# Optimization experiments

Hardware: AMD Instinct MI355X
Metric: run time of the kernel (lower is better)

## Reference

```python
import jax, jax.numpy as jnp
import numpy as np

B, S, D = 4, 2048, 512
H = 8
DEPTH = D // H  # 64


def setup_inputs() -> dict:
    key = jax.random.key(0)
    ks = jax.random.split(key, 6)
    scale = 1.0 / np.sqrt(D)
    return {
        "x": jax.random.normal(ks[0], (B, S, D), dtype=jnp.float32),
        "y": jax.random.normal(ks[1], (B, S, D), dtype=jnp.float32),
        "W_q": jax.random.normal(ks[2], (D, D), dtype=jnp.float32) * scale,
        "W_k": jax.random.normal(ks[3], (D, D), dtype=jnp.float32) * scale,
        "W_v": jax.random.normal(ks[4], (D, D), dtype=jnp.float32) * scale,
        "W_o": jax.random.normal(ks[5], (D, D), dtype=jnp.float32) * scale,
    }


def _split_heads(t):
    # [B, S, D] -> [B, H, S, DEPTH]
    b, s, _ = t.shape
    return t.reshape(b, s, H, DEPTH).transpose(0, 2, 1, 3)


def reference(x, y, W_q, W_k, W_v, W_o):
    q = _split_heads(x @ W_q) * (DEPTH ** -0.5)   # [B,H,Sq,d]
    k = _split_heads(y @ W_k)                      # [B,H,Sk,d]
    v = _split_heads(y @ W_v)                      # [B,H,Sk,d]
    logits = jnp.einsum("bhqd,bhkd->bhqk", q, k)   # [B,H,Sq,Sk]
    weights = jax.nn.softmax(logits, axis=-1)
    attn = jnp.einsum("bhqk,bhkd->bhqd", weights, v)  # [B,H,Sq,d]
    attn = attn.transpose(0, 2, 1, 3).reshape(x.shape[0], x.shape[1], D)
    return attn @ W_o
```

## Files before the change

### kernel.cpp

```cpp
#include <hip/hip_runtime.h>
#include <hip/hip_bf16.h>
#include <math.h>
#include <stdint.h>

#define NB 4
#define NS 2048
#define ND 512
#define NH 8
#define DEP 64

typedef __attribute__((ext_vector_type(8))) short bf16x8;
typedef __attribute__((ext_vector_type(4))) short bf16x4;
typedef __attribute__((ext_vector_type(4))) float f32x4;

#define QSCALE 0.18033688011112042f

__device__ __forceinline__ short f2b(float f) {
  unsigned u = __float_as_uint(f);
  u += 0x7FFF + ((u >> 16) & 1);
  return (short)(u >> 16);
}
__device__ __forceinline__ unsigned pk2(float a, float b) {
  union { __hip_bfloat162 h; unsigned u; } c;
  c.h = __float22bfloat162_rn(float2{a, b});
  return c.u;
}
__device__ __forceinline__ void dma16(const void* g, void* l) {
  __builtin_amdgcn_global_load_lds(
      (const __attribute__((address_space(1))) void*)g,
      (__attribute__((address_space(3))) void*)l, 16, 0, 0);
}

__global__ __launch_bounds__(256) void prep(
    const float* __restrict__ x, const float* __restrict__ y,
    const float* __restrict__ W0, const float* __restrict__ W1,
    const float* __restrict__ W2, const float* __restrict__ W3,
    short* __restrict__ xb, short* __restrict__ yb, short* __restrict__ T0,
    short* __restrict__ T1, short* __restrict__ T2, short* __restrict__ T3) {
  const int t = threadIdx.x;
  if (blockIdx.y < 2) {
    const float* src = blockIdx.y ? y : x;
    short* dst = blockIdx.y ? yb : xb;
    size_t i = ((size_t)blockIdx.x * 256 + t) * 4;
    float4 v = *(const float4*)(src + i);
    bf16x4 o;
    o[0] = f2b(v.x); o[1] = f2b(v.y); o[2] = f2b(v.z); o[3] = f2b(v.w);
    *(bf16x4*)(dst + i) = o;
    return;
  }
  const int bx = blockIdx.x;
  if (bx >= 256) return;
  const int wj = bx >> 6, rem = bx & 63;
  const float* W = wj == 0 ? W0 : wj == 1 ? W1 : wj == 2 ? W2 : W3;
  short* T = wj == 0 ? T0 : wj == 1 ? T1 : wj == 2 ? T2 : T3;
  __shared__ float tile[64][65];
  const int k0 = (rem >> 3) * 64, n0 = (rem & 7) * 64;
#pragma unroll
  for (int i = 0; i < 4; ++i) {
    int r = (t >> 4) + i * 16;
    int c = (t & 15) * 4;
    float4 v = *(const float4*)&W[(size_t)(k0 + r) * ND + n0 + c];
    tile[r][c] = v.x; tile[r][c + 1] = v.y;
    tile[r][c + 2] = v.z; tile[r][c + 3] = v.w;
  }
  __syncthreads();
#pragma unroll
  for (int i = 0; i < 4; ++i) {
    int n = (t >> 4) + i * 16;
    int kc = (t & 15) * 4;
    bf16x4 o;
#pragma unroll
    for (int j = 0; j < 4; ++j) o[j] = f2b(tile[kc + j][n]);
    *(bf16x4*)&T[(size_t)(n0 + n) * ND + k0 + kc] = o;
  }
}

__global__ __launch_bounds__(256) void qkv_gemm(
    const short* __restrict__ xb, const short* __restrict__ yb,
    const short* __restrict__ Wqt, const short* __restrict__ Wkt,
    const short* __restrict__ Wvt, short* __restrict__ Qb,
    short* __restrict__ Kb, short* __restrict__ Vtb) {
  __shared__ short As[128 * 64];
  __shared__ short B0s[64 * 64];
  __shared__ short B1s[64 * 64];
  const int z = blockIdx.z;
  const short* A = z ? yb : xb;
  const short* Bt0 = z ? Wkt : Wqt;
  const int t = threadIdx.x;
  const int wave = t >> 6, lane = t & 63;
  const int m = lane & 15, quad = lane >> 4;
  const int m0 = blockIdx.y * 128, n0 = blockIdx.x * 64;
  const int mh = (wave >> 1) * 64, nh = (wave & 1) * 32;
  const int r8 = lane >> 3;
  const int c8 = (lane & 7) ^ r8;
  const int mx7 = m & 7;
  f32x4 acc0[4][2], acc1[4][2];
#pragma unroll
  for (int i = 0; i < 4; ++i)
#pragma unroll
    for (int j = 0; j < 2; ++j) {
      acc0[i][j] = (f32x4){0.f, 0.f, 0.f, 0.f};
      acc1[i][j] = (f32x4){0.f, 0.f, 0.f, 0.f};
    }

  for (int k0 = 0; k0 < ND; k0 += 64) {
    __syncthreads();
#pragma unroll
    for (int i = 0; i < 4; ++i)
      dma16(A + (size_t)(m0 + i * 32 + wave * 8 + r8) * ND + k0 + c8 * 8,
            As + (i * 256 + wave * 64) * 8);
#pragma unroll
    for (int i = 0; i < 2; ++i)
      dma16(Bt0 + (size_t)(n0 + i * 32 + wave * 8 + r8) * ND + k0 + c8 * 8,
            B0s + (i * 256 + wave * 64) * 8);
    if (z) {
#pragma unroll
      for (int i = 0; i < 2; ++i)
        dma16(Wvt + (size_t)(n0 + i * 32 + wave * 8 + r8) * ND + k0 + c8 * 8,
              B1s + (i * 256 + wave * 64) * 8);
    }
    __syncthreads();
    bf16x8 af[4][2], bf0[2][2];
#pragma unroll
    for (int mt = 0; mt < 4; ++mt)
#pragma unroll
      for (int kc = 0; kc < 2; ++kc)
        af[mt][kc] = *(const bf16x8*)(As + (mh + mt * 16 + m) * 64 +
                                      ((kc * 4 + quad) ^ mx7) * 8);
#pragma unroll
    for (int nt = 0; nt < 2; ++nt)
#pragma unroll
      for (int kc = 0; kc < 2; ++kc)
        bf0[nt][kc] = *(const bf16x8*)(B0s + (nh + nt * 16 + m) * 64 +
                                       ((kc * 4 + quad) ^ mx7) * 8);
#pragma unroll
    for (int mt = 0; mt < 4; ++mt)
#pragma unroll
      for (int nt = 0; nt < 2; ++nt)
#pragma unroll
        for (int kc = 0; kc < 2; ++kc)
          acc0[mt][nt] = __builtin_amdgcn_mfma_f32_16x16x32_bf16(
              af[mt][kc], bf0[nt][kc], acc0[mt][nt], 0, 0, 0);
    if (z) {
      bf16x8 bf1[2][2];
#pragma unroll
      for (int nt = 0; nt < 2; ++nt)
#pragma unroll
        for (int kc = 0; kc < 2; ++kc)
          bf1[nt][kc] = *(const bf16x8*)(B1s + (nh + nt * 16 + m) * 64 +
                                         ((kc * 4 + quad) ^ mx7) * 8);
#pragma unroll
      for (int mt = 0; mt < 4; ++mt)
#pragma unroll
        for (int nt = 0; nt < 2; ++nt)
#pragma unroll
          for (int kc = 0; kc < 2; ++kc)
            acc1[mt][nt] = __builtin_amdgcn_mfma_f32_16x16x32_bf16(
                af[mt][kc], bf1[nt][kc], acc1[mt][nt], 0, 0, 0);
    }
  }
  short* C0 = z ? Kb : Qb;
  const float alpha0 = z ? 1.0f : QSCALE;
#pragma unroll
  for (int mt = 0; mt < 4; ++mt)
#pragma unroll
    for (int nt = 0; nt < 2; ++nt)
#pragma unroll
      for (int r = 0; r < 4; ++r) {
        int row = m0 + mh + mt * 16 + quad * 4 + r;
        int col = n0 + nh + nt * 16 + m;
        C0[(size_t)row * ND + col] = f2b(acc0[mt][nt][r] * alpha0);
      }
  if (z) {
#pragma unroll
    for (int mt = 0; mt < 4; ++mt)
#pragma unroll
      for (int nt = 0; nt < 2; ++nt) {
        int row0 = m0 + mh + mt * 16 + quad * 4;
        int col = n0 + nh + nt * 16 + m;
        int b_ = row0 >> 11, s_ = row0 & (NS - 1);
        int h_ = col >> 6, d_ = col & (DEP - 1);
        uint2 p;
        p.x = pk2(acc1[mt][nt][0], acc1[mt][nt][1]);
        p.y = pk2(acc1[mt][nt][2], acc1[mt][nt][3]);
        *(uint2*)(Vtb + (size_t)((b_ * NH + h_) * DEP + d_) * NS + s_) = p;
      }
  }
}

__global__ __launch_bounds__(256) void out_gemm(const short* __restrict__ A,
                                                const short* __restrict__ Bt,
                                                float* __restrict__ Cout) {
  __shared__ short As[2][128 * 64];
  __shared__ short Bs[2][64 * 64];
  const int t = threadIdx.x;
  const int wave = t >> 6, lane = t & 63;
  const int m = lane & 15, quad = lane >> 4;
  const int m0 = blockIdx.y * 128, n0 = blockIdx.x * 64;
  const int mh = (wave >> 1) * 64, nh = (wave & 1) * 32;
  const int r8 = lane >> 3;
  const int c8 = (lane & 7) ^ r8;
  const int mx7 = m & 7;
  f32x4 acc[4][2];
#pragma unroll
  for (int i = 0; i < 4; ++i)
#pragma unroll
    for (int j = 0; j < 2; ++j) acc[i][j] = (f32x4){0.f, 0.f, 0.f, 0.f};

#pragma unroll
  for (int i = 0; i < 4; ++i)
    dma16(A + (size_t)(m0 + i * 32 + wave * 8 + r8) * ND + c8 * 8,
          As[0] + (i * 256 + wave * 64) * 8);
#pragma unroll
  for (int i = 0; i < 2; ++i)
    dma16(Bt + (size_t)(n0 + i * 32 + wave * 8 + r8) * ND + c8 * 8,
          Bs[0] + (i * 256 + wave * 64) * 8);

  int buf = 0;
  for (int k0 = 0; k0 < ND; k0 += 64, buf ^= 1) {
    __syncthreads();
    if (k0 + 64 < ND) {
#pragma unroll
      for (int i = 0; i < 4; ++i)
        dma16(A + (size_t)(m0 + i * 32 + wave * 8 + r8) * ND + k0 + 64 + c8 * 8,
              As[buf ^ 1] + (i * 256 + wave * 64) * 8);
#pragma unroll
      for (int i = 0; i < 2; ++i)
        dma16(Bt + (size_t)(n0 + i * 32 + wave * 8 + r8) * ND + k0 + 64 +
                  c8 * 8,
              Bs[buf ^ 1] + (i * 256 + wave * 64) * 8);
    }
    bf16x8 af[4][2], bf[2][2];
#pragma unroll
    for (int mt = 0; mt < 4; ++mt)
#pragma unroll
      for (int kc = 0; kc < 2; ++kc)
        af[mt][kc] = *(const bf16x8*)(As[buf] + (mh + mt * 16 + m) * 64 +
                                      ((kc * 4 + quad) ^ mx7) * 8);
#pragma unroll
    for (int nt = 0; nt < 2; ++nt)
#pragma unroll
      for (int kc = 0; kc < 2; ++kc)
        bf[nt][kc] = *(const bf16x8*)(Bs[buf] + (nh + nt * 16 + m) * 64 +
                                      ((kc * 4 + quad) ^ mx7) * 8);
#pragma unroll
    for (int mt = 0; mt < 4; ++mt)
#pragma unroll
      for (int nt = 0; nt < 2; ++nt)
#pragma unroll
        for (int kc = 0; kc < 2; ++kc)
          acc[mt][nt] = __builtin_amdgcn_mfma_f32_16x16x32_bf16(
              af[mt][kc], bf[nt][kc], acc[mt][nt], 0, 0, 0);
  }
#pragma unroll
  for (int mt = 0; mt < 4; ++mt)
#pragma unroll
    for (int nt = 0; nt < 2; ++nt)
#pragma unroll
      for (int r = 0; r < 4; ++r) {
        int row = m0 + mh + mt * 16 + quad * 4 + r;
        int col = n0 + nh + nt * 16 + m;
        Cout[(size_t)row * ND + col] = acc[mt][nt][r];
      }
}

__global__ __launch_bounds__(256) void attn_mfma(const short* __restrict__ Qb,
                                                 const short* __restrict__ Kb,
                                                 const short* __restrict__ Vtb,
                                                 short* __restrict__ Ob) {
  __shared__ short Ks[2][64 * 64];
  __shared__ short Vts[2][64 * 64];
  __shared__ short Pt[64 * 64];
  const int t = threadIdx.x;
  const int wave = t >> 6, lane = t & 63;
  const int m = lane & 15, quad = lane >> 4;
  const int kh = wave >> 1, qh = wave & 1;
  const int bh = blockIdx.y, b = bh >> 3, h = bh & 7;
  const int q0 = blockIdx.x * 64;
  const size_t rowb = (size_t)b * NS;
  const short* Vtbase = Vtb + (size_t)(bh * DEP) * NS;
  const int r8 = lane >> 3;
  const int c8 = (lane & 7) ^ r8;
  const int mx7 = m & 7;

  bf16x8 qf[2][2];
#pragma unroll
  for (int nt = 0; nt < 2; ++nt)
#pragma unroll
    for (int kc = 0; kc < 2; ++kc)
      qf[nt][kc] =
          *(const bf16x8*)(Qb + (rowb + q0 + qh * 32 + nt * 16 + m) * ND +
                           h * DEP + kc * 32 + quad * 8);

  float l_[2] = {0.0f, 0.0f};
  f32x4 Ot[4][2];
#pragma unroll
  for (int mt = 0; mt < 4; ++mt)
#pragma unroll
    for (int nt = 0; nt < 2; ++nt) Ot[mt][nt] = (f32x4){0.f, 0.f, 0.f, 0.f};

#pragma unroll
  for (int i = 0; i < 2; ++i) {
    int row = i * 32 + wave * 8 + r8;
    dma16(Kb + (rowb + row) * ND + h * DEP + c8 * 8,
          Ks[0] + (i * 256 + wave * 64) * 8);
    dma16(Vtbase + (size_t)row * NS + c8 * 8,
          Vts[0] + (i * 256 + wave * 64) * 8);
  }

  int buf = 0;
  for (int kv0 = 0; kv0 < NS; kv0 += 64, buf ^= 1) {
    __syncthreads();
    if (kv0 + 64 < NS) {
#pragma unroll
      for (int i = 0; i < 2; ++i) {
        int row = i * 32 + wave * 8 + r8;
        dma16(Kb + (rowb + kv0 + 64 + row) * ND + h * DEP + c8 * 8,
              Ks[buf ^ 1] + (i * 256 + wave * 64) * 8);
        dma16(Vtbase + (size_t)row * NS + kv0 + 64 + c8 * 8,
              Vts[buf ^ 1] + (i * 256 + wave * 64) * 8);
      }
    }

    f32x4 St[2][2];
#pragma unroll
    for (int mt = 0; mt < 2; ++mt)
#pragma unroll
      for (int nt = 0; nt < 2; ++nt) St[mt][nt] = (f32x4){0.f, 0.f, 0.f, 0.f};
#pragma unroll
    for (int mt = 0; mt < 2; ++mt)
#pragma unroll
      for (int kc = 0; kc < 2; ++kc) {
        bf16x8 kf =
            *(const bf16x8*)(Ks[buf] + (kh * 32 + mt * 16 + m) * 64 +
                             ((kc * 4 + quad) ^ mx7) * 8);
#pragma unroll
        for (int nt = 0; nt < 2; ++nt)
          St[mt][nt] = __builtin_amdgcn_mfma_f32_16x16x32_bf16(
              kf, qf[nt][kc], St[mt][nt], 0, 0, 0);
      }

#pragma unroll
    for (int nt = 0; nt < 2; ++nt) {
      float rs = 0.0f;
#pragma unroll
      for (int mt = 0; mt < 2; ++mt) {
        float p0 = __builtin_amdgcn_exp2f(St[mt][nt][0]);
        float p1 = __builtin_amdgcn_exp2f(St[mt][nt][1]);
        float p2 = __builtin_amdgcn_exp2f(St[mt][nt][2]);
        float p3 = __builtin_amdgcn_exp2f(St[mt][nt][3]);
        rs += (p0 + p1) + (p2 + p3);
        uint2 pk;
        pk.x = pk2(p0, p1);
        pk.y = pk2(p2, p3);
        *(uint2*)(Pt + (qh * 32 + nt * 16 + m) * 64 +
                  ((kh * 4 + mt * 2 + (quad >> 1)) ^ mx7) * 8 +
                  (quad & 1) * 4) = pk;
      }
      l_[nt] += rs;
    }

#pragma unroll
    for (int nt = 0; nt < 2; ++nt) {
      bf16x8 pf = *(const bf16x8*)(Pt + (qh * 32 + nt * 16 + m) * 64 +
                                   ((kh * 4 + quad) ^ mx7) * 8);
#pragma unroll
      for (int mt = 0; mt < 4; ++mt) {
        bf16x8 vf = *(const bf16x8*)(Vts[buf] + (mt * 16 + m) * 64 +
                                     ((kh * 4 + quad) ^ mx7) * 8);
        Ot[mt][nt] = __builtin_amdgcn_mfma_f32_16x16x32_bf16(vf, pf, Ot[mt][nt],
                                                             0, 0, 0);
      }
    }
  }

#pragma unroll
  for (int nt = 0; nt < 2; ++nt) {
    l_[nt] += __shfl_xor(l_[nt], 16, 64);
    l_[nt] += __shfl_xor(l_[nt], 32, 64);
  }
  float* obuf = (float*)Ks;
  float* lv = (float*)Vts;
  if (kh == 1) {
    float* dst = obuf + (qh * 64 + lane) * 32;
#pragma unroll
    for (int mt = 0; mt < 4; ++mt)
#pragma unroll
      for (int nt = 0; nt < 2; ++nt)
#pragma unroll
        for (int r = 0; r < 4; ++r) dst[mt * 8 + nt * 4 + r] = Ot[mt][nt][r];
    if (quad == 0) {
      lv[qh * 32 + m] = l_[0];
      lv[qh * 32 + 16 + m] = l_[1];
    }
  }
  __syncthreads();
  if (kh == 0) {
    const float* src = obuf + (qh * 64 + lane) * 32;
    float linv[2];
#pragma unroll
    for (int nt = 0; nt < 2; ++nt)
      linv[nt] = 1.0f / (l_[nt] + lv[qh * 32 + nt * 16 + m]);
#pragma unroll
    for (int nt = 0; nt < 2; ++nt) {
      size_t row = rowb + q0 + qh * 32 + nt * 16 + m;
#pragma unroll
      for (int mt = 0; mt < 4; ++mt) {
        float v0 = (Ot[mt][nt][0] + src[mt * 8 + nt * 4 + 0]) * linv[nt];
        float v1 = (Ot[mt][nt][1] + src[mt * 8 + nt * 4 + 1]) * linv[nt];
        float v2 = (Ot[mt][nt][2] + src[mt * 8 + nt * 4 + 2]) * linv[nt];
        float v3 = (Ot[mt][nt][3] + src[mt * 8 + nt * 4 + 3]) * linv[nt];
        uint2 p;
        p.x = pk2(v0, v1);
        p.y = pk2(v2, v3);
        *(uint2*)(Ob + row * ND + h * DEP + mt * 16 + quad * 4) = p;
      }
    }
  }
}

extern "C" void kernel_launch(void* const* d_in, const int* in_sizes, int n_in,
                              void* d_out, int out_size, void* d_ws,
                              size_t ws_size, hipStream_t stream) {
  const float* x = (const float*)d_in[0];
  const float* y = (const float*)d_in[1];
  const float* Wq = (const float*)d_in[2];
  const float* Wk = (const float*)d_in[3];
  const float* Wv = (const float*)d_in[4];
  const float* Wo = (const float*)d_in[5];
  float* out = (float*)d_out;

  const size_t mat = (size_t)NB * NS * ND;
  const size_t wsz = (size_t)ND * ND;
  short* xb = (short*)d_ws;
  short* yb = xb + mat;
  short* Wqt = yb + mat;
  short* Wkt = Wqt + wsz;
  short* Wvt = Wkt + wsz;
  short* Wot = Wvt + wsz;
  short* Qb = Wot + wsz;
  short* Kb = Qb + mat;
  short* Vtb = Kb + mat;
  short* attnb = xb;

  prep<<<dim3(mat / 1024, 3), 256, 0, stream>>>(x, y, Wq, Wk, Wv, Wo, xb, yb,
                                                Wqt, Wkt, Wvt, Wot);
  qkv_gemm<<<dim3(ND / 64, (NB * NS) / 128, 2), 256, 0, stream>>>(
      xb, yb, Wqt, Wkt, Wvt, Qb, Kb, Vtb);
  attn_mfma<<<dim3(NS / 64, NB * NH), 256, 0, stream>>>(Qb, Kb, Vtb, attnb);
  out_gemm<<<dim3(ND / 64, (NB * NS) / 128), 256, 0, stream>>>(attnb, Wot,
                                                               out);
}
```

Measured before the change: 201.1 us.

## Switch attention kernel to 32x32x16 MFMA tiles with new LDS swizzle

Rewrites the attention inner loop to use 32x32x16 bf16 MFMA instead of 16x16x32, so each wave owns a 32x32 score tile and a 32-row output tile. LDS swizzle patterns for K, V^T and P are redone to match the new fragment layout, and the row-sum reduction needs one shuffle instead of two. The larger MFMA shape means fewer instructions and fragment loads per tile. The cost is larger accumulators (32 floats of output per lane) and an extra barrier before the cross-wave merge.

```diff
diff --git a/kernel.cpp b/kernel.cpp
--- a/kernel.cpp
+++ b/kernel.cpp
@@ -12,6 +12,7 @@
 typedef __attribute__((ext_vector_type(8))) short bf16x8;
 typedef __attribute__((ext_vector_type(4))) short bf16x4;
 typedef __attribute__((ext_vector_type(4))) float f32x4;
+typedef __attribute__((ext_vector_type(16))) float f32x16;
 
 #define QSCALE 0.18033688011112042f
 
@@ -273,34 +274,34 @@
   __shared__ short Pt[64 * 64];
   const int t = threadIdx.x;
   const int wave = t >> 6, lane = t & 63;
-  const int m = lane & 15, quad = lane >> 4;
+  const int n32 = lane & 31, l5 = lane >> 5;
   const int kh = wave >> 1, qh = wave & 1;
   const int bh = blockIdx.y, b = bh >> 3, h = bh & 7;
   const int q0 = blockIdx.x * 64;
   const size_t rowb = (size_t)b * NS;
   const short* Vtbase = Vtb + (size_t)(bh * DEP) * NS;
   const int r8 = lane >> 3;
-  const int c8 = (lane & 7) ^ r8;
-  const int mx7 = m & 7;
-
-  bf16x8 qf[2][2];
-#pragma unroll
-  for (int nt = 0; nt < 2; ++nt)
-#pragma unroll
-    for (int kc = 0; kc < 2; ++kc)
-      qf[nt][kc] =
-          *(const bf16x8*)(Qb + (rowb + q0 + qh * 32 + nt * 16 + m) * ND +
-                           h * DEP + kc * 32 + quad * 8);
-
-  float l_[2] = {0.0f, 0.0f};
-  f32x4 Ot[4][2];
-#pragma unroll
-  for (int mt = 0; mt < 4; ++mt)
-#pragma unroll
-    for (int nt = 0; nt < 2; ++nt) Ot[mt][nt] = (f32x4){0.f, 0.f, 0.f, 0.f};
+  const int qrow = qh * 32 + n32;
+  const int swf = (n32 ^ (n32 >> 3)) & 7;
+  const int swk = swf ^ (kh << 2);
+  const int swq = (qrow ^ (qrow >> 3)) & 7;
+
+  bf16x8 qf[4];
+#pragma unroll
+  for (int kc = 0; kc < 4; ++kc)
+    qf[kc] = *(const bf16x8*)(Qb + (rowb + q0 + qrow) * ND + h * DEP +
+                              kc * 16 + l5 * 8);
+
+  float l_ = 0.0f;
+  f32x16 Ot[2];
+#pragma unroll
+  for (int mt = 0; mt < 2; ++mt)
+#pragma unroll
+    for (int r = 0; r < 16; ++r) Ot[mt][r] = 0.0f;
 
 #pragma unroll
   for (int i = 0; i < 2; ++i) {
+    int c8 = (lane & 7) ^ (r8 ^ ((i * 4 + wave) & 7));
     int row = i * 32 + wave * 8 + r8;
     dma16(Kb + (rowb + row) * ND + h * DEP + c8 * 8,
           Ks[0] + (i * 256 + wave * 64) * 8);
@@ -314,6 +315,7 @@
     if (kv0 + 64 < NS) {
 #pragma unroll
       for (int i = 0; i < 2; ++i) {
+        int c8 = (lane & 7) ^ (r8 ^ ((i * 4 + wave) & 7));
         int row = i * 32 + wave * 8 + r8;
         dma16(Kb + (rowb + kv0 + 64 + row) * ND + h * DEP + c8 * 8,
               Ks[buf ^ 1] + (i * 256 + wave * 64) * 8);
@@ -322,100 +324,78 @@
       }
     }
 
-    f32x4 St[2][2];
-#pragma unroll
-    for (int mt = 0; mt < 2; ++mt)
-#pragma unroll
-      for (int nt = 0; nt < 2; ++nt) St[mt][nt] = (f32x4){0.f, 0.f, 0.f, 0.f};
-#pragma unroll
-    for (int mt = 0; mt < 2; ++mt)
-#pragma unroll
-      for (int kc = 0; kc < 2; ++kc) {
-        bf16x8 kf =
-            *(const bf16x8*)(Ks[buf] + (kh * 32 + mt * 16 + m) * 64 +
-                             ((kc * 4 + quad) ^ mx7) * 8);
-#pragma unroll
-        for (int nt = 0; nt < 2; ++nt)
-          St[mt][nt] = __builtin_amdgcn_mfma_f32_16x16x32_bf16(
-              kf, qf[nt][kc], St[mt][nt], 0, 0, 0);
-      }
-
-#pragma unroll
-    for (int nt = 0; nt < 2; ++nt) {
-      float rs = 0.0f;
+    f32x16 St;
+#pragma unroll
+    for (int r = 0; r < 16; ++r) St[r] = 0.0f;
+#pragma unroll
+    for (int kc = 0; kc < 4; ++kc) {
+      bf16x8 kf = *(const bf16x8*)(Ks[buf] + (kh * 32 + n32) * 64 +
+                                   ((kc * 2 + l5) ^ swk) * 8);
+      St = __builtin_amdgcn_mfma_f32_32x32x16_bf16(kf, qf[kc], St, 0, 0, 0);
+    }
+
+    float p[16];
+    float rs = 0.0f;
+#pragma unroll
+    for (int r = 0; r < 16; ++r) {
+      p[r] = __builtin_amdgcn_exp2f(St[r]);
+      rs += p[r];
+    }
+    l_ += rs;
+#pragma unroll
+    for (int r4 = 0; r4 < 4; ++r4) {
+      uint2 pk;
+      pk.x = pk2(p[r4 * 4 + 0], p[r4 * 4 + 1]);
+      pk.y = pk2(p[r4 * 4 + 2], p[r4 * 4 + 3]);
+      *(uint2*)(Pt + qrow * 64 + ((kh * 4 + r4) ^ swq) * 8 + l5 * 4) = pk;
+    }
+
+#pragma unroll
+    for (int kc = 0; kc < 2; ++kc) {
+      bf16x8 pf = *(const bf16x8*)(Pt + qrow * 64 +
+                                   ((kh * 4 + kc * 2 + l5) ^ swq) * 8);
 #pragma unroll
       for (int mt = 0; mt < 2; ++mt) {
-        float p0 = __builtin_amdgcn_exp2f(St[mt][nt][0]);
-        float p1 = __builtin_amdgcn_exp2f(St[mt][nt][1]);
-        float p2 = __builtin_amdgcn_exp2f(St[mt][nt][2]);
-        float p3 = __builtin_amdgcn_exp2f(St[mt][nt][3]);
-        rs += (p0 + p1) + (p2 + p3);
-        uint2 pk;
-        pk.x = pk2(p0, p1);
-        pk.y = pk2(p2, p3);
-        *(uint2*)(Pt + (qh * 32 + nt * 16 + m) * 64 +
-                  ((kh * 4 + mt * 2 + (quad >> 1)) ^ mx7) * 8 +
-                  (quad & 1) * 4) = pk;
-      }
-      l_[nt] += rs;
-    }
-
-#pragma unroll
-    for (int nt = 0; nt < 2; ++nt) {
-      bf16x8 pf = *(const bf16x8*)(Pt + (qh * 32 + nt * 16 + m) * 64 +
-                                   ((kh * 4 + quad) ^ mx7) * 8);
-#pragma unroll
-      for (int mt = 0; mt < 4; ++mt) {
-        bf16x8 vf = *(const bf16x8*)(Vts[buf] + (mt * 16 + m) * 64 +
-                                     ((kh * 4 + quad) ^ mx7) * 8);
-        Ot[mt][nt] = __builtin_amdgcn_mfma_f32_16x16x32_bf16(vf, pf, Ot[mt][nt],
-                                                             0, 0, 0);
-      }
-    }
-  }
-
-#pragma unroll
-  for (int nt = 0; nt < 2; ++nt) {
-    l_[nt] += __shfl_xor(l_[nt], 16, 64);
-    l_[nt] += __shfl_xor(l_[nt], 32, 64);
-  }
+        bf16x8 vf = *(const bf16x8*)(Vts[buf] + (mt * 32 + n32) * 64 +
+                                     ((kh * 4 + kc * 2 + l5) ^ swf ^
+                                      (mt << 2)) * 8);
+        Ot[mt] =
+            __builtin_amdgcn_mfma_f32_32x32x16_bf16(vf, pf, Ot[mt], 0, 0, 0);
+      }
+    }
+  }
+
+  l_ += __shfl_xor(l_, 32, 64);
+  __syncthreads();
   float* obuf = (float*)Ks;
   float* lv = (float*)Vts;
   if (kh == 1) {
     float* dst = obuf + (qh * 64 + lane) * 32;
 #pragma unroll
-    for (int mt = 0; mt < 4; ++mt)
-#pragma unroll
-      for (int nt = 0; nt < 2; ++nt)
-#pragma unroll
-        for (int r = 0; r < 4; ++r) dst[mt * 8 + nt * 4 + r] = Ot[mt][nt][r];
-    if (quad == 0) {
-      lv[qh * 32 + m] = l_[0];
-      lv[qh * 32 + 16 + m] = l_[1];
-    }
+    for (int mt = 0; mt < 2; ++mt)
+#pragma unroll
+      for (int r = 0; r < 16; ++r) dst[mt * 16 + r] = Ot[mt][r];
+    lv[qh * 64 + lane] = l_;
   }
   __syncthreads();
   if (kh == 0) {
     const float* src = obuf + (qh * 64 + lane) * 32;
-    float linv[2];
-#pragma unroll
-    for (int nt = 0; nt < 2; ++nt)
-      linv[nt] = 1.0f / (l_[nt] + lv[qh * 32 + nt * 16 + m]);
-#pragma unroll
-    for (int nt = 0; nt < 2; ++nt) {
-      size_t row = rowb + q0 + qh * 32 + nt * 16 + m;
-#pragma unroll
-      for (int mt = 0; mt < 4; ++mt) {
-        float v0 = (Ot[mt][nt][0] + src[mt * 8 + nt * 4 + 0]) * linv[nt];
-        float v1 = (Ot[mt][nt][1] + src[mt * 8 + nt * 4 + 1]) * linv[nt];
-        float v2 = (Ot[mt][nt][2] + src[mt * 8 + nt * 4 + 2]) * linv[nt];
-        float v3 = (Ot[mt][nt][3] + src[mt * 8 + nt * 4 + 3]) * linv[nt];
-        uint2 p;
-        p.x = pk2(v0, v1);
-        p.y = pk2(v2, v3);
-        *(uint2*)(Ob + row * ND + h * DEP + mt * 16 + quad * 4) = p;
-      }
-    }
+    float linv = 1.0f / (l_ + lv[qh * 64 + lane]);
+    size_t grow = rowb + q0 + qrow;
+#pragma unroll
+    for (int mt = 0; mt < 2; ++mt)
+#pragma unroll
+      for (int r4 = 0; r4 < 4; ++r4) {
+        int d = mt * 32 + 8 * r4 + 4 * l5;
+        float v0 = (Ot[mt][r4 * 4 + 0] + src[mt * 16 + r4 * 4 + 0]) * linv;
+        float v1 = (Ot[mt][r4 * 4 + 1] + src[mt * 16 + r4 * 4 + 1]) * linv;
+        float v2 = (Ot[mt][r4 * 4 + 2] + src[mt * 16 + r4 * 4 + 2]) * linv;
+        float v3 = (Ot[mt][r4 * 4 + 3] + src[mt * 16 + r4 * 4 + 3]) * linv;
+        uint2 o;
+        o.x = pk2(v0, v1);
+        o.y = pk2(v2, v3);
+        *(uint2*)(Ob + grow * ND + h * DEP + d) = o;
+      }
   }
 }
 
```

After: 190.2 us. 5.4% less time.
